# Kernel tuning notes

Measured on AMD Instinct MI355X. Metric: run time of the kernel, lower is better.

Reference implementation:

```python
import jax, jax.numpy as jnp
import numpy as np

N = 1_000_000
LIMS = ((0.0, 51.2), (-25.6, 25.6), (-2.0, 4.4))
SIZES = (256, 256, 32)
GM = np.array([0.2, 0.2, 0.2], np.float32)      # grid_meters
MINS = np.array([0.0, -25.6, -2.0], np.float32)  # xmin, ymin, zmin
OFFSET = 0.5
INIT = 32  # init_size; VFE units = INIT // 2 = 16


def setup_inputs() -> dict:
    key = jax.random.key(0)
    ks = jax.random.split(key, 20)
    lo = jnp.array([l[0] for l in LIMS], jnp.float32)
    hi = jnp.array([l[1] for l in LIMS], jnp.float32)
    # keep points strictly inside lims so quantized idx stays in range
    u = jax.random.uniform(ks[0], (N, 3), minval=1e-3, maxval=1.0 - 1e-3)
    xyz = lo + (hi - lo) * u
    inten = jax.random.uniform(ks[1], (N, 1))
    pc = jnp.concatenate([xyz, inten], axis=1).astype(jnp.float32)
    indicator = jnp.array([0, N // 2, N], jnp.int32)

    def lin(k, o, i):
        return (0.02 * jax.random.normal(k, (o, i), jnp.float32))

    def bias(k, o):
        return (0.02 * jax.random.normal(k, (o,), jnp.float32))

    U = INIT // 2  # 16, VFE units (last_vfe=False)
    return dict(
        pc=pc, indicator=indicator,
        w05=lin(ks[2], U, 10), b05=bias(ks[3], U),
        ww05=lin(ks[4], U, 6), wb05=bias(ks[5], U),
        w1=lin(ks[6], U, 10), b1=bias(ks[7], U),
        ww1=lin(ks[8], U, 6), wb1=bias(ks[9], U),
        am_w=lin(ks[10], INIT, 6), am_b=bias(ks[11], INIT),
        at_w=lin(ks[12], INIT, 2 * INIT), at_b=bias(ks[13], INIT),
        af_w=lin(ks[14], INIT, INIT), af_b=bias(ks[15], INIT),
    )


def _unique_inverse(ids):
    # emulate torch.unique(dim=0, return_inverse=True) via sort+rank on linear voxel ids
    n = ids.shape[0]
    order = jnp.argsort(ids)
    s = ids[order]
    new = jnp.concatenate([jnp.zeros((1,), jnp.int32), (s[1:] != s[:-1]).astype(jnp.int32)])
    ranks = jnp.cumsum(new)
    return jnp.zeros((n,), jnp.int32).at[order].set(ranks)


def _voxel_coords(pc, indicator, scale):
    n = pc.shape[0]
    B = indicator.shape[0] - 1
    bt = jnp.repeat(jnp.arange(B, dtype=jnp.int32), jnp.diff(indicator), total_repeat_length=n)
    nx = int(SIZES[0] // scale); ny = int(SIZES[1] // scale); nz = int(SIZES[2] // scale)
    def quant(col, lim, size):
        idx = (col - lim[0]) / (lim[1] - lim[0]) * float(size)
        return idx.astype(jnp.int32)
    xi = quant(pc[:, 0], LIMS[0], nx)
    yi = quant(pc[:, 1], LIMS[1], ny)
    zi = quant(pc[:, 2], LIMS[2], nz)
    coords = jnp.stack([bt, xi, yi, zi], axis=-1)  # [n,4] bxyz_indx
    lid = ((bt * nx + xi) * ny + yi) * nz + zi     # lexicographic-consistent linear id
    return coords, lid


def _scale_features(pc, coords, inv, Wl, bl, Ww, bw):
    # add_pcmean_and_gridmean + VFELayerMinus (activate=False, gs=None)
    n = pc.shape[0]
    cnt = jax.ops.segment_sum(jnp.ones((n,), jnp.float32), inv, num_segments=n)
    pc_mean = jax.ops.segment_sum(pc[:, :3], inv, num_segments=n) / jnp.maximum(cnt, 1.0)[:, None]
    mm = pc[:, :3] - pc_mean[inv]                                   # pc_mean_minus
    gm = jnp.asarray(GM); mins = jnp.asarray(MINS)
    gmm = pc[:, :3] - ((coords[:, 1:].astype(jnp.float32) + OFFSET) * gm + mins)  # pc_gridmean_minus
    feat = jnp.concatenate([pc, mm, gmm], axis=1)   # [n,10]
    mean = jnp.concatenate([mm, gmm], axis=1)       # [n,6]
    x = feat @ Wl.T + bl                            # [n,16]
    x = x * (mean @ Ww.T + bw)
    mx = jax.ops.segment_max(x, inv, num_segments=n)
    return jnp.concatenate([x, mx[inv]], axis=1), mean  # [n,32], [n,6]


def reference(pc, indicator, w05, b05, ww05, wb05, w1, b1, ww1, wb1,
              am_w, am_b, at_w, at_b, af_w, af_b):
    n = pc.shape[0]
    coords05, lid05 = _voxel_coords(pc, indicator, 0.5)
    coords1, lid1 = _voxel_coords(pc, indicator, 1)
    inv05 = _unique_inverse(lid05)
    inv1 = _unique_inverse(lid1)
    f05, _ = _scale_features(pc, coords05, inv05, w05, b05, ww05, wb05)
    f1, mean1 = _scale_features(pc, coords1, inv1, w1, b1, ww1, wb1)
    agg = jax.nn.relu(mean1 @ am_w.T + am_b) * \
          jax.nn.relu(jnp.concatenate([f05, f1], axis=1) @ at_w.T + at_b)
    agg = agg @ af_w.T + af_b                       # [n,32]
    maxf = jax.ops.segment_max(agg, inv1, num_segments=n)
    cnt = jax.ops.segment_sum(jnp.ones((n,), jnp.float32), inv1, num_segments=n)
    maxf = jnp.where(cnt[:, None] > 0, maxf, 0.0)   # pad empty rows (torch output has no such rows)
    coord_ind = jnp.zeros((n, 4), jnp.int32).at[inv1].set(coords1)  # unique coords, padded to n
    return maxf, coord_ind, inv1
```

## Files before the change

kernel.cpp:

```cpp
#include <hip/hip_runtime.h>
#include <cstdint>
#include <cstdio>


struct Coords { int xi, yi, zi; };

__device__ __forceinline__ Coords quantc(float x, float y, float z, float sx, float sy, float sz) {
    Coords c;
    c.xi = (int)(((x - 0.0f)  / 51.2f) * sx);
    c.yi = (int)(((y + 25.6f) / 51.2f) * sy);
    c.zi = (int)(((z + 2.0f)  / 6.4f)  * sz);
    return c;
}

__device__ __forceinline__ int batch_of(int i, const int* __restrict__ ind, int B) {
    int bt = 0;
    for (int b = 1; b < B; ++b) if (i >= ind[b]) bt = b;
    return bt;
}

__device__ __forceinline__ unsigned f2o(float f) {
    unsigned u = __float_as_uint(f);
    return (u & 0x80000000u) ? ~u : (u | 0x80000000u);
}
__device__ __forceinline__ float o2f(unsigned u) {
    return (u & 0x80000000u) ? __uint_as_float(u ^ 0x80000000u) : __uint_as_float(~u);
}
#define NEG_O 0x007FFFFFu

__device__ __forceinline__ unsigned short f2bf(float x) {
    unsigned u = __float_as_uint(x);
    unsigned r = (u + 0x7FFFu + ((u >> 16) & 1u)) >> 16;
    return (unsigned short)r;
}
__device__ __forceinline__ float bf2f(unsigned h) {
    return __uint_as_float(h << 16);
}

__device__ __forceinline__ void compute_x16(
    float px, float py, float pz, float pw,
    float mx_, float my_, float mz_, Coords c,
    const float* __restrict__ W, const float* __restrict__ Bv,
    const float* __restrict__ Ww, const float* __restrict__ Wb,
    float* __restrict__ x, float* __restrict__ mean6) {
    float gx = px - (((float)c.xi + 0.5f) * 0.2f + 0.0f);
    float gy = py - (((float)c.yi + 0.5f) * 0.2f + (-25.6f));
    float gz = pz - (((float)c.zi + 0.5f) * 0.2f + (-2.0f));
    float mmx = px - mx_, mmy = py - my_, mmz = pz - mz_;
    float feat[10] = {px, py, pz, pw, mmx, mmy, mmz, gx, gy, gz};
    float mean[6]  = {mmx, mmy, mmz, gx, gy, gz};
#pragma unroll
    for (int j = 0; j < 6; ++j) mean6[j] = mean[j];
#pragma unroll
    for (int o = 0; o < 16; ++o) {
        float a = Bv[o];
#pragma unroll
        for (int j = 0; j < 10; ++j) a += feat[j] * W[o * 10 + j];
        float g = Wb[o];
#pragma unroll
        for (int j = 0; j < 6; ++j) g += mean[j] * Ww[o * 6 + j];
        x[o] = a * g;
    }
}


__global__ __launch_bounds__(256) void k_bits(
    const float4* __restrict__ pc, const int* __restrict__ ind, int B, int n,
    unsigned* __restrict__ mask05, unsigned* __restrict__ mask1) {
    int i = blockIdx.x * 256 + threadIdx.x;
    if (i >= n) return;
    float4 p = pc[i];
    int bt = batch_of(i, ind, B);
    Coords c05 = quantc(p.x, p.y, p.z, 512.f, 512.f, 64.f);
    Coords c1  = quantc(p.x, p.y, p.z, 256.f, 256.f, 32.f);
    int lid05 = ((bt * 512 + c05.xi) * 512 + c05.yi) * 64 + c05.zi;
    int lid1  = ((bt * 256 + c1.xi)  * 256 + c1.yi)  * 32 + c1.zi;
    atomicOr(&mask05[lid05 >> 5], 1u << (lid05 & 31));
    atomicOr(&mask1[lid1 >> 5],  1u << (lid1 & 31));
}

__global__ __launch_bounds__(256) void k_wtr(
    const float* __restrict__ at_w, const float* __restrict__ af_w,
    const float* __restrict__ am_w,
    float* __restrict__ atT, float* __restrict__ afT, float* __restrict__ amT) {
    int i = blockIdx.x * 256 + threadIdx.x;
    if (i < 2048) {
        int o = i >> 6, c = i & 63;
        atT[c * 32 + o] = at_w[i];
    } else if (i < 3072) {
        int j = i - 2048; int o = j >> 5, q = j & 31;
        afT[q * 32 + o] = af_w[j];
    } else if (i < 3264) {
        int j = i - 3072; int o = j / 6, q = j % 6;
        amT[q * 32 + o] = am_w[j];
    }
}

__global__ __launch_bounds__(256) void k_chunk2(
    const unsigned* __restrict__ maskA, unsigned* __restrict__ bsumA, int nWA, int nBA,
    const unsigned* __restrict__ maskB, unsigned* __restrict__ bsumB, int nWB) {
    const unsigned* mask; unsigned* bsum; int nW, blk;
    if ((int)blockIdx.x < nBA) { mask = maskA; bsum = bsumA; nW = nWA; blk = blockIdx.x; }
    else { mask = maskB; bsum = bsumB; nW = nWB; blk = blockIdx.x - nBA; }
    int t = threadIdx.x;
    int base = blk * 2048 + t;
    unsigned tot = 0;
#pragma unroll
    for (int k = 0; k < 8; ++k) {
        int w = base + k * 256;
        if (w < nW) tot += __popc(mask[w]);
    }
    __shared__ unsigned s[256];
    s[t] = tot;
    __syncthreads();
    for (int off = 128; off > 0; off >>= 1) {
        if (t < off) s[t] += s[t + off];
        __syncthreads();
    }
    if (t == 0) bsum[blk] = s[0];
}

__global__ __launch_bounds__(256) void k_chunku2(
    const unsigned* __restrict__ cntA, unsigned* __restrict__ bsumA,
    const unsigned* __restrict__ cntB, unsigned* __restrict__ bsumB,
    int nElem, int nCh) {
    const unsigned* val; unsigned* bsum; int blk;
    if ((int)blockIdx.x < nCh) { val = cntA; bsum = bsumA; blk = blockIdx.x; }
    else { val = cntB; bsum = bsumB; blk = blockIdx.x - nCh; }
    int t = threadIdx.x;
    int base = blk * 2048 + t;
    unsigned tot = 0;
#pragma unroll
    for (int k = 0; k < 8; ++k) {
        int w = base + k * 256;
        if (w < nElem) tot += val[w];
    }
    __shared__ unsigned s[256];
    s[t] = tot;
    __syncthreads();
    for (int off = 128; off > 0; off >>= 1) {
        if (t < off) s[t] += s[t + off];
        __syncthreads();
    }
    if (t == 0) bsum[blk] = s[0];
}

__global__ __launch_bounds__(1024) void k_scan2(
    const unsigned* __restrict__ bsumA, unsigned* __restrict__ bprefA,
    unsigned* __restrict__ UoutA, int nA,
    const unsigned* __restrict__ bsumB, unsigned* __restrict__ bprefB,
    unsigned* __restrict__ UoutB, int nB) {
    const unsigned* bsum; unsigned* bpref; unsigned* Uout; int nBn;
    if (blockIdx.x == 0) { bsum = bsumA; bpref = bprefA; Uout = UoutA; nBn = nA; }
    else { bsum = bsumB; bpref = bprefB; Uout = UoutB; nBn = nB; }
    __shared__ unsigned s[1024];
    int t = threadIdx.x;
    int ipt = (nBn + 1023) >> 10;
    unsigned tot = 0;
    for (int k = 0; k < ipt; ++k) {
        int e = t * ipt + k;
        if (e < nBn) tot += bsum[e];
    }
    s[t] = tot;
    __syncthreads();
    for (int off = 1; off < 1024; off <<= 1) {
        unsigned v = 0;
        if (t >= off) v = s[t - off];
        __syncthreads();
        if (t >= off) s[t] += v;
        __syncthreads();
    }
    unsigned run = s[t] - tot;
    for (int k = 0; k < ipt; ++k) {
        int e = t * ipt + k;
        if (e < nBn) { bpref[e] = run; run += bsum[e]; }
    }
    if (t == 1023 && Uout) *Uout = s[1023];
}

__global__ __launch_bounds__(256) void k_wpref2(
    const unsigned* __restrict__ maskA, const unsigned* __restrict__ bprefA,
    unsigned* __restrict__ wprefA, int nWA, int nBA,
    const unsigned* __restrict__ maskB, const unsigned* __restrict__ bprefB,
    unsigned* __restrict__ wprefB, int nWB) {
    const unsigned* mask; const unsigned* bpref; unsigned* wpref; int nW, blk;
    if ((int)blockIdx.x < nBA) { mask = maskA; bpref = bprefA; wpref = wprefA; nW = nWA; blk = blockIdx.x; }
    else { mask = maskB; bpref = bprefB; wpref = wprefB; nW = nWB; blk = blockIdx.x - nBA; }
    int t = threadIdx.x;
    int base = blk * 2048 + t * 8;
    unsigned p[8];
    unsigned tot = 0;
#pragma unroll
    for (int k = 0; k < 8; ++k) {
        int w = base + k;
        p[k] = (w < nW) ? __popc(mask[w]) : 0u;
        tot += p[k];
    }
    __shared__ unsigned s[256];
    s[t] = tot;
    __syncthreads();
    for (int off = 1; off < 256; off <<= 1) {
        unsigned v = 0;
        if (t >= off) v = s[t - off];
        __syncthreads();
        if (t >= off) s[t] += v;
        __syncthreads();
    }
    unsigned run = bpref[blk] + (s[t] - tot);
#pragma unroll
    for (int k = 0; k < 8; ++k) {
        int w = base + k;
        if (w < nW) { wpref[w] = run; run += p[k]; }
    }
}

__global__ __launch_bounds__(256) void k_eprefu2(
    const unsigned* __restrict__ cntA, const unsigned* __restrict__ bprefA,
    unsigned* __restrict__ startA,
    const unsigned* __restrict__ cntB, const unsigned* __restrict__ bprefB,
    unsigned* __restrict__ startB,
    int nElem, int nCh) {
    const unsigned* val; const unsigned* bpref; unsigned* epref; int blk;
    if ((int)blockIdx.x < nCh) { val = cntA; bpref = bprefA; epref = startA; blk = blockIdx.x; }
    else { val = cntB; bpref = bprefB; epref = startB; blk = blockIdx.x - nCh; }
    int t = threadIdx.x;
    int base = blk * 2048 + t * 8;
    unsigned p[8];
    unsigned tot = 0;
#pragma unroll
    for (int k = 0; k < 8; ++k) {
        int w = base + k;
        p[k] = (w < nElem) ? val[w] : 0u;
        tot += p[k];
    }
    __shared__ unsigned s[256];
    s[t] = tot;
    __syncthreads();
    for (int off = 1; off < 256; off <<= 1) {
        unsigned v = 0;
        if (t >= off) v = s[t - off];
        __syncthreads();
        if (t >= off) s[t] += v;
        __syncthreads();
    }
    unsigned run = bpref[blk] + (s[t] - tot);
#pragma unroll
    for (int k = 0; k < 8; ++k) {
        int w = base + k;
        if (w < nElem) { epref[w] = run; run += p[k]; }
    }
}


__global__ __launch_bounds__(256) void k_rank(
    const float4* __restrict__ pc, const int* __restrict__ ind, int B, int n,
    const unsigned* __restrict__ mask05, const unsigned* __restrict__ wp05,
    const unsigned* __restrict__ mask1, const unsigned* __restrict__ wp1,
    unsigned* __restrict__ inv05, unsigned* __restrict__ inv1,
    unsigned* __restrict__ cnt05, unsigned* __restrict__ cnt1,
    unsigned* __restrict__ slot05, unsigned* __restrict__ slot1,
    float* __restrict__ outCoord, float* __restrict__ outInv) {
    int i = blockIdx.x * 256 + threadIdx.x;
    if (i >= n) return;
    float4 p = pc[i];
    int bt = batch_of(i, ind, B);
    Coords c05 = quantc(p.x, p.y, p.z, 512.f, 512.f, 64.f);
    Coords c1  = quantc(p.x, p.y, p.z, 256.f, 256.f, 32.f);
    int lid05 = ((bt * 512 + c05.xi) * 512 + c05.yi) * 64 + c05.zi;
    int lid1  = ((bt * 256 + c1.xi)  * 256 + c1.yi)  * 32 + c1.zi;

    unsigned w = (unsigned)lid05 >> 5, b = (unsigned)lid05 & 31u;
    unsigned r05 = wp05[w] + __popc(mask05[w] & ((1u << b) - 1u));
    w = (unsigned)lid1 >> 5; b = (unsigned)lid1 & 31u;
    unsigned r1 = wp1[w] + __popc(mask1[w] & ((1u << b) - 1u));

    inv05[i] = r05;
    inv1[i] = r1;
    outInv[i] = (float)r1;

    slot05[i] = atomicAdd(&cnt05[r05], 1u);
    unsigned sl1 = atomicAdd(&cnt1[r1], 1u);
    slot1[i] = sl1;
    if (sl1 == 0u)
        ((float4*)outCoord)[r1] = make_float4((float)bt, (float)c1.xi, (float)c1.yi, (float)c1.zi);
}

__global__ __launch_bounds__(256) void k_slot(
    const float4* __restrict__ pc,
    const unsigned* __restrict__ inv05, const unsigned* __restrict__ inv1,
    const unsigned* __restrict__ slot05, const unsigned* __restrict__ slot1,
    const unsigned* __restrict__ start05, const unsigned* __restrict__ start1,
    const unsigned* __restrict__ cnt1,
    uint4* __restrict__ recA05, uint4* __restrict__ recA1, int n) {
    int i = blockIdx.x * 256 + threadIdx.x;
    if (i >= n) return;
    float4 p = pc[i];
    unsigned r05 = inv05[i], r1 = inv1[i];
    unsigned p05 = start05[r05] + slot05[i];
    unsigned s1 = start1[r1];
    unsigned p1  = s1 + slot1[i];
    unsigned c1 = cnt1[r1];
    unsigned cm = c1 < 257u ? c1 : 257u;
    unsigned meta = s1 | (cm << 23);
    uint4 pw = *(const uint4*)&p;
    recA05[(size_t)p05 * 2]     = pw;
    recA05[(size_t)p05 * 2 + 1] = make_uint4(r05, 0u, 0u, 0u);
    recA1[(size_t)p1 * 2]       = pw;
    recA1[(size_t)p1 * 2 + 1]   = make_uint4(r1, r05, meta, 0u);
}

__global__ __launch_bounds__(256) void k_segmean2(
    const uint4* __restrict__ recA05, const unsigned* __restrict__ start05,
    const unsigned* __restrict__ cnt05, float4* __restrict__ mean05,
    const uint4* __restrict__ recA1, const unsigned* __restrict__ start1,
    const unsigned* __restrict__ cnt1, float4* __restrict__ mean1,
    unsigned char* __restrict__ flags, unsigned* __restrict__ outMaxU,
    int n, int gpts) {
    if ((int)blockIdx.x >= 2 * gpts) {
        int blk3 = blockIdx.x - 2 * gpts;
        int b = blk3 * 256 + threadIdx.x + 1;
        if (b >= gpts) return;
        int j = b * 256;
        if (j >= n) return;
        unsigned r = recA1[(size_t)j * 2 + 1].x;
        if (start1[r] < (unsigned)j) {
            flags[r] = 1;
            unsigned* row = outMaxU + (size_t)r * 32;
#pragma unroll
            for (int o = 0; o < 32; ++o) row[o] = NEG_O;
        }
        return;
    }
    const uint4* recA; const unsigned* start; const unsigned* cnt;
    float4* meanOut; int blk;
    if ((int)blockIdx.x < gpts) {
        recA = recA05; start = start05; cnt = cnt05; meanOut = mean05; blk = blockIdx.x;
    } else {
        recA = recA1; start = start1; cnt = cnt1; meanOut = mean1; blk = blockIdx.x - gpts;
    }
    int j = blk * 256 + threadIdx.x;
    int lane = threadIdx.x & 63;
    bool live = j < n;
    unsigned r = 0xFFFFFFFFu;
    float sx = 0.f, sy = 0.f, sz = 0.f;
    if (live) {
        float4 p = *(const float4*)&recA[(size_t)j * 2];
        r = recA[(size_t)j * 2 + 1].x;
        sx = p.x; sy = p.y; sz = p.z;
    }
#pragma unroll
    for (int d = 1; d < 64; d <<= 1) {
        unsigned rn = (unsigned)__shfl_down((int)r, d);
        float ax = __shfl_down(sx, d);
        float ay = __shfl_down(sy, d);
        float az = __shfl_down(sz, d);
        bool ok = (lane + d) < 64 && rn == r;
        if (ok) { sx += ax; sy += ay; sz += az; }
    }
    if (!live) return;
    if (j != (int)start[r]) return;
    unsigned c = cnt[r];
    unsigned end = j + c;
    unsigned waveEnd = ((unsigned)j & ~63u) + 64u;
    for (unsigned j2 = waveEnd; j2 < end; ++j2) {
        float4 q = *(const float4*)&recA[(size_t)j2 * 2];
        sx += q.x; sy += q.y; sz += q.z;
    }
    float cf = (float)c;
    meanOut[r] = make_float4(sx / cf, sy / cf, sz / cf, 0.f);
}

__global__ __launch_bounds__(256) void k_segmx2(
    const uint4* __restrict__ recA05, const unsigned* __restrict__ start05,
    const unsigned* __restrict__ cnt05, const float4* __restrict__ mean05,
    const float* __restrict__ w05, const float* __restrict__ b05,
    const float* __restrict__ ww05, const float* __restrict__ wb05,
    unsigned short* __restrict__ mx05,
    const uint4* __restrict__ recA1, const unsigned* __restrict__ start1,
    const unsigned* __restrict__ cnt1, const float4* __restrict__ mean1,
    const float* __restrict__ w1, const float* __restrict__ b1,
    const float* __restrict__ ww1, const float* __restrict__ wb1,
    unsigned short* __restrict__ mx1,
    int n, int gpts) {
    const uint4* recA; const unsigned* start; const unsigned* cnt;
    const float4* meanIn; const float* W; const float* Bv; const float* Ww;
    const float* Wb; unsigned short* mxOut; int blk;
    float sx_, sy_, sz_;
    if ((int)blockIdx.x < gpts) {
        recA = recA05; start = start05; cnt = cnt05; meanIn = mean05;
        W = w05; Bv = b05; Ww = ww05; Wb = wb05; mxOut = mx05;
        sx_ = 512.f; sy_ = 512.f; sz_ = 64.f; blk = blockIdx.x;
    } else {
        recA = recA1; start = start1; cnt = cnt1; meanIn = mean1;
        W = w1; Bv = b1; Ww = ww1; Wb = wb1; mxOut = mx1;
        sx_ = 256.f; sy_ = 256.f; sz_ = 32.f; blk = blockIdx.x - gpts;
    }
    __shared__ float buf[256][17];
    int t = threadIdx.x;
    int j = blk * 256 + t;
    bool live = j < n;
    unsigned r = 0;
    float x[16], d6[6];
    if (live) {
        float4 p = *(const float4*)&recA[(size_t)j * 2];
        r = recA[(size_t)j * 2 + 1].x;
        float4 mv = meanIn[r];
        Coords cc = quantc(p.x, p.y, p.z, sx_, sy_, sz_);
        compute_x16(p.x, p.y, p.z, p.w, mv.x, mv.y, mv.z, cc, W, Bv, Ww, Wb, x, d6);
    } else {
#pragma unroll
        for (int o = 0; o < 16; ++o) x[o] = 0.f;
    }
#pragma unroll
    for (int o = 0; o < 16; ++o) buf[t][o] = x[o];
    __syncthreads();
    if (!live || j != (int)start[r]) return;
    unsigned c = cnt[r];
    unsigned end = j + c;
    unsigned blockEnd = ((unsigned)blk + 1u) * 256u;
    unsigned inEnd = end < blockEnd ? end : blockEnd;
    for (unsigned j2 = j + 1; j2 < inEnd; ++j2) {
        int t2 = t + (int)(j2 - (unsigned)j);
#pragma unroll
        for (int o = 0; o < 16; ++o) x[o] = fmaxf(x[o], buf[t2][o]);
    }
    float4 mv = meanIn[r];
    for (unsigned j2 = blockEnd; j2 < end; ++j2) {
        float4 q = *(const float4*)&recA[(size_t)j2 * 2];
        Coords cc = quantc(q.x, q.y, q.z, sx_, sy_, sz_);
        float x2[16];
        compute_x16(q.x, q.y, q.z, q.w, mv.x, mv.y, mv.z, cc, W, Bv, Ww, Wb, x2, d6);
#pragma unroll
        for (int o = 0; o < 16; ++o) x[o] = fmaxf(x[o], x2[o]);
    }
    unsigned pk[8];
#pragma unroll
    for (int k = 0; k < 8; ++k)
        pk[k] = (unsigned)f2bf(x[2 * k]) | ((unsigned)f2bf(x[2 * k + 1]) << 16);
    uint4* mr = (uint4*)(mxOut + (size_t)r * 16);
    mr[0] = make_uint4(pk[0], pk[1], pk[2], pk[3]);
    mr[1] = make_uint4(pk[4], pk[5], pk[6], pk[7]);
}

__global__ __launch_bounds__(256, 3) void k_val(
    const uint4* __restrict__ recA1,
    const float4* __restrict__ mean05, const unsigned short* __restrict__ mx05,
    const float4* __restrict__ mean1, const unsigned short* __restrict__ mx1,
    const float* __restrict__ w05, const float* __restrict__ b05,
    const float* __restrict__ ww05, const float* __restrict__ wb05,
    const float* __restrict__ w1g, const float* __restrict__ b1g,
    const float* __restrict__ ww1, const float* __restrict__ wb1,
    const float* __restrict__ amT, const float* __restrict__ am_b,
    const float* __restrict__ atT, const float* __restrict__ at_b,
    const float* __restrict__ afT, const float* __restrict__ af_b,
    float* __restrict__ outMax, int n) {
    __shared__ float buf[256][17];
    int t = threadIdx.x;
    int j = blockIdx.x * 256 + t;
    bool live = j < n;
    unsigned r = 0, s = 0, c = 0;
    bool bound = false;
    float2 at2[16];
    if (live) {
        uint4 pw4 = recA1[(size_t)j * 2];
        float4 p = *(const float4*)&pw4;
        uint4 mw = recA1[(size_t)j * 2 + 1];
        r = mw.x;
        unsigned r05 = mw.y;
        unsigned meta = mw.z;
        s = meta & 0x7FFFFFu;
        c = meta >> 23;
        bound = (c > 256u) || ((s >> 8) != ((s + c - 1) >> 8));

#pragma unroll
        for (int k = 0; k < 16; ++k) at2[k] = ((const float2*)at_b)[k];

        {
            const uint4* m4 = (const uint4*)(mx1 + (size_t)r * 16);
            uint4 a = m4[0], b2 = m4[1];
            unsigned pw[8] = {a.x, a.y, a.z, a.w, b2.x, b2.y, b2.z, b2.w};
#pragma unroll
            for (int kk = 0; kk < 8; ++kk) {
                float e0 = bf2f(pw[kk] & 0xFFFFu);
                float e1 = bf2f(pw[kk] >> 16);
                const float2* wc0 = (const float2*)(atT + (48 + 2 * kk) * 32);
                const float2* wc1 = (const float2*)(atT + (49 + 2 * kk) * 32);
#pragma unroll
                for (int k = 0; k < 16; ++k) {
                    float2 w0 = wc0[k], w1 = wc1[k];
                    at2[k].x += e0 * w0.x + e1 * w1.x;
                    at2[k].y += e0 * w0.y + e1 * w1.y;
                }
            }
        }
        {
            const uint4* m4 = (const uint4*)(mx05 + (size_t)r05 * 16);
            uint4 a = m4[0], b2 = m4[1];
            unsigned pw[8] = {a.x, a.y, a.z, a.w, b2.x, b2.y, b2.z, b2.w};
#pragma unroll
            for (int kk = 0; kk < 8; ++kk) {
                float e0 = bf2f(pw[kk] & 0xFFFFu);
                float e1 = bf2f(pw[kk] >> 16);
                const float2* wc0 = (const float2*)(atT + (16 + 2 * kk) * 32);
                const float2* wc1 = (const float2*)(atT + (17 + 2 * kk) * 32);
#pragma unroll
                for (int k = 0; k < 16; ++k) {
                    float2 w0 = wc0[k], w1 = wc1[k];
                    at2[k].x += e0 * w0.x + e1 * w1.x;
                    at2[k].y += e0 * w0.y + e1 * w1.y;
                }
            }
        }
        {
            float4 mv = mean05[r05];
            Coords cc = quantc(p.x, p.y, p.z, 512.f, 512.f, 64.f);
            float gx = p.x - (((float)cc.xi + 0.5f) * 0.1f + 0.0f);
            float gy = p.y - (((float)cc.yi + 0.5f) * 0.1f + (-25.6f));
            float gz = p.z - (((float)cc.zi + 0.5f) * 0.1f + (-2.0f));
            float mmx = p.x - mv.x, mmy = p.y - mv.y, mmz = p.z - mv.z;
            float feat[10] = {p.x, p.y, p.z, p.w, mmx, mmy, mmz, gx, gy, gz};
#pragma unroll
            for (int jj = 0; jj < 16; ++jj) {
                float a_ = b05[jj];
#pragma unroll
                for (int q = 0; q < 10; ++q) a_ += feat[q] * w05[jj * 10 + q];
                float g_ = wb05[jj];
#pragma unroll
                for (int q = 0; q < 6; ++q) g_ += feat[4 + q] * ww05[jj * 6 + q];
                float x_ = a_ * g_;
                const float2* wc = (const float2*)(atT + jj * 32);
#pragma unroll
                for (int k = 0; k < 16; ++k) {
                    float2 w0 = wc[k];
                    at2[k].x += x_ * w0.x;
                    at2[k].y += x_ * w0.y;
                }
            }
        }
        float mean6[6];
        {
            float4 mv = mean1[r];
            Coords cc = quantc(p.x, p.y, p.z, 256.f, 256.f, 32.f);
            float gx = p.x - (((float)cc.xi + 0.5f) * 0.2f + 0.0f);
            float gy = p.y - (((float)cc.yi + 0.5f) * 0.2f + (-25.6f));
            float gz = p.z - (((float)cc.zi + 0.5f) * 0.2f + (-2.0f));
            float mmx = p.x - mv.x, mmy = p.y - mv.y, mmz = p.z - mv.z;
            float feat[10] = {p.x, p.y, p.z, p.w, mmx, mmy, mmz, gx, gy, gz};
            mean6[0] = mmx; mean6[1] = mmy; mean6[2] = mmz;
            mean6[3] = gx;  mean6[4] = gy;  mean6[5] = gz;
#pragma unroll
            for (int jj = 0; jj < 16; ++jj) {
                float a_ = b1g[jj];
#pragma unroll
                for (int q = 0; q < 10; ++q) a_ += feat[q] * w1g[jj * 10 + q];
                float g_ = wb1[jj];
#pragma unroll
                for (int q = 0; q < 6; ++q) g_ += feat[4 + q] * ww1[jj * 6 + q];
                float x_ = a_ * g_;
                const float2* wc = (const float2*)(atT + (32 + jj) * 32);
#pragma unroll
                for (int k = 0; k < 16; ++k) {
                    float2 w0 = wc[k];
                    at2[k].x += x_ * w0.x;
                    at2[k].y += x_ * w0.y;
                }
            }
        }
        {
            float2 am2[16];
#pragma unroll
            for (int k = 0; k < 16; ++k) am2[k] = ((const float2*)am_b)[k];
#pragma unroll
            for (int q = 0; q < 6; ++q) {
                float m = mean6[q];
                const float2* wc = (const float2*)(amT + q * 32);
#pragma unroll
                for (int k = 0; k < 16; ++k) {
                    float2 w0 = wc[k];
                    am2[k].x += m * w0.x;
                    am2[k].y += m * w0.y;
                }
            }
#pragma unroll
            for (int k = 0; k < 16; ++k) {
                at2[k].x = fmaxf(am2[k].x, 0.f) * fmaxf(at2[k].x, 0.f);
                at2[k].y = fmaxf(am2[k].y, 0.f) * fmaxf(at2[k].y, 0.f);
            }
        }
    } else {
#pragma unroll
        for (int k = 0; k < 16; ++k) at2[k] = make_float2(0.f, 0.f);
    }

    float ats[32];
#pragma unroll
    for (int k = 0; k < 16; ++k) { ats[2 * k] = at2[k].x; ats[2 * k + 1] = at2[k].y; }

    bool owner = live && !bound && (j == (int)s);
    unsigned end = s + c;
    unsigned* arow = (unsigned*)outMax + (size_t)r * 32;
    float4* ov = (float4*)(outMax + (size_t)r * 32);

    if (live) {
#pragma unroll
        for (int k = 0; k < 8; ++k) {
            float2 v2 = ((const float2*)af_b)[k];
#pragma unroll
            for (int q = 0; q < 32; ++q) {
                float aq = ats[q];
                float2 w2 = ((const float2*)(afT + q * 32))[k];
                v2.x += aq * w2.x;
                v2.y += aq * w2.y;
            }
            if (bound) {
                atomicMax(&arow[2 * k], f2o(v2.x));
                atomicMax(&arow[2 * k + 1], f2o(v2.y));
            } else {
                buf[t][2 * k] = v2.x;
                buf[t][2 * k + 1] = v2.y;
            }
        }
    }
    __syncthreads();
    if (owner) {
        float vm[16];
#pragma unroll
        for (int o = 0; o < 16; ++o) vm[o] = buf[t][o];
        for (unsigned j2 = (unsigned)j + 1; j2 < end; ++j2) {
            int t2 = t + (int)(j2 - (unsigned)j);
#pragma unroll
            for (int o = 0; o < 16; ++o) vm[o] = fmaxf(vm[o], buf[t2][o]);
        }
#pragma unroll
        for (int k = 0; k < 4; ++k)
            ov[k] = make_float4(vm[4 * k], vm[4 * k + 1], vm[4 * k + 2], vm[4 * k + 3]);
    }
    __syncthreads();
    if (live) {
#pragma unroll
        for (int k = 8; k < 16; ++k) {
            float2 v2 = ((const float2*)af_b)[k];
#pragma unroll
            for (int q = 0; q < 32; ++q) {
                float aq = ats[q];
                float2 w2 = ((const float2*)(afT + q * 32))[k];
                v2.x += aq * w2.x;
                v2.y += aq * w2.y;
            }
            if (bound) {
                atomicMax(&arow[2 * k], f2o(v2.x));
                atomicMax(&arow[2 * k + 1], f2o(v2.y));
            } else {
                buf[t][2 * (k - 8)] = v2.x;
                buf[t][2 * (k - 8) + 1] = v2.y;
            }
        }
    }
    __syncthreads();
    if (owner) {
        float vm[16];
#pragma unroll
        for (int o = 0; o < 16; ++o) vm[o] = buf[t][o];
        for (unsigned j2 = (unsigned)j + 1; j2 < end; ++j2) {
            int t2 = t + (int)(j2 - (unsigned)j);
#pragma unroll
            for (int o = 0; o < 16; ++o) vm[o] = fmaxf(vm[o], buf[t2][o]);
        }
#pragma unroll
        for (int k = 0; k < 4; ++k)
            ov[4 + k] = make_float4(vm[4 * k], vm[4 * k + 1], vm[4 * k + 2], vm[4 * k + 3]);
    }
}

__global__ __launch_bounds__(256) void k_finrow(
    float* __restrict__ outMax, float* __restrict__ outCoord,
    const unsigned char* __restrict__ flags, const unsigned* __restrict__ U1p, int n) {
    int idx = blockIdx.x * 256 + threadIdx.x;
    if (idx >= n * 8) return;
    int r = idx >> 3, k = idx & 7;
    unsigned U = *U1p;
    if ((unsigned)r >= U) {
        float4 z = make_float4(0.f, 0.f, 0.f, 0.f);
        ((float4*)outMax)[idx] = z;
        if (k == 0) ((float4*)outCoord)[r] = z;
    } else if (flags[r]) {
        unsigned* u4 = (unsigned*)outMax + (size_t)idx * 4;
        float* f4 = outMax + (size_t)idx * 4;
#pragma unroll
        for (int o = 0; o < 4; ++o) f4[o] = o2f(u4[o]);
    }
}


extern "C" void kernel_launch(void* const* d_in, const int* in_sizes, int n_in,
                              void* d_out, int out_size, void* d_ws, size_t ws_size,
                              hipStream_t stream) {
    const float4* pc = (const float4*)d_in[0];
    const int* ind   = (const int*)d_in[1];
    const float* w05 = (const float*)d_in[2];
    const float* b05 = (const float*)d_in[3];
    const float* ww05 = (const float*)d_in[4];
    const float* wb05 = (const float*)d_in[5];
    const float* w1  = (const float*)d_in[6];
    const float* b1  = (const float*)d_in[7];
    const float* ww1 = (const float*)d_in[8];
    const float* wb1 = (const float*)d_in[9];
    const float* am_w = (const float*)d_in[10];
    const float* am_b = (const float*)d_in[11];
    const float* at_w = (const float*)d_in[12];
    const float* at_b = (const float*)d_in[13];
    const float* af_w = (const float*)d_in[14];
    const float* af_b = (const float*)d_in[15];

    int n = in_sizes[0] / 4;
    int B = in_sizes[1] - 1;

    int nW05 = B * (512 * 512 * 64 / 32);
    int nW1  = B * (256 * 256 * 32 / 32);
    int nB05 = (nW05 + 2047) / 2048;
    int nB1  = (nW1 + 2047) / 2048;
    int nCh  = (n + 2047) / 2048;

    size_t off = 0;
    char* base = (char*)d_ws;
    auto take = [&](size_t bytes) -> char* {
        char* p = base + off;
        off = (off + bytes + 255) & ~(size_t)255;
        return p;
    };

    unsigned* mask05 = (unsigned*)take((size_t)nW05 * 4);
    unsigned* mask1  = (unsigned*)take((size_t)nW1 * 4);
    unsigned* cnt05  = (unsigned*)take((size_t)n * 4);
    unsigned* cnt1   = (unsigned*)take((size_t)n * 4);
    unsigned char* flags = (unsigned char*)take((size_t)n);
    size_t zeroBytes = off;

    unsigned* wp05   = (unsigned*)take((size_t)nW05 * 4);
    unsigned* wp1    = (unsigned*)take((size_t)nW1 * 4);
    unsigned* inv05  = (unsigned*)take((size_t)n * 4);
    unsigned* inv1   = (unsigned*)take((size_t)n * 4);
    unsigned* slot05 = (unsigned*)take((size_t)n * 4);
    unsigned* slot1  = (unsigned*)take((size_t)n * 4);
    unsigned* start05 = (unsigned*)take((size_t)n * 4);
    unsigned* start1  = (unsigned*)take((size_t)n * 4);
    uint4*    recA05  = (uint4*)take((size_t)n * 32);
    uint4*    recA1   = (uint4*)take((size_t)n * 32);
    float4*   mean05  = (float4*)take((size_t)n * 16);
    float4*   mean1   = (float4*)take((size_t)n * 16);
    unsigned short* mx05 = (unsigned short*)take((size_t)n * 32);
    unsigned short* mx1  = (unsigned short*)take((size_t)n * 32);
    float*    atT     = (float*)take((size_t)2048 * 4);
    float*    afT     = (float*)take((size_t)1024 * 4);
    float*    amT     = (float*)take((size_t)192 * 4);
    unsigned* bsum05  = (unsigned*)take((size_t)nB05 * 4);
    unsigned* bpref05 = (unsigned*)take((size_t)nB05 * 4);
    unsigned* bsum1   = (unsigned*)take((size_t)nB1 * 4);
    unsigned* bpref1  = (unsigned*)take((size_t)nB1 * 4);
    unsigned* bsC05   = (unsigned*)take((size_t)nCh * 4);
    unsigned* bpC05   = (unsigned*)take((size_t)nCh * 4);
    unsigned* bsC1    = (unsigned*)take((size_t)nCh * 4);
    unsigned* bpC1    = (unsigned*)take((size_t)nCh * 4);
    unsigned* U1p     = (unsigned*)take(4);
    size_t total = off;

    if (ws_size < total) {
        fprintf(stderr, "kernel_launch: ws too small (%zu < %zu)\n", ws_size, total);
        return;
    }

    float* outMaxF = (float*)d_out;
    float* outCoord = (float*)d_out + (size_t)n * 32;
    float* outInv = (float*)d_out + (size_t)n * 36;

    hipMemsetAsync(d_ws, 0, zeroBytes, stream);

    int gpts = (n + 255) / 256;
    int nbb  = (gpts + 255) / 256;
    k_wtr<<<13, 256, 0, stream>>>(at_w, af_w, am_w, atT, afT, amT);
    k_bits<<<gpts, 256, 0, stream>>>(pc, ind, B, n, mask05, mask1);
    k_chunk2<<<nB05 + nB1, 256, 0, stream>>>(mask05, bsum05, nW05, nB05,
                                             mask1, bsum1, nW1);
    k_scan2<<<2, 1024, 0, stream>>>(bsum05, bpref05, nullptr, nB05,
                                    bsum1, bpref1, U1p, nB1);
    k_wpref2<<<nB05 + nB1, 256, 0, stream>>>(mask05, bpref05, wp05, nW05, nB05,
                                             mask1, bpref1, wp1, nW1);
    k_rank<<<gpts, 256, 0, stream>>>(pc, ind, B, n, mask05, wp05, mask1, wp1,
                                     inv05, inv1, cnt05, cnt1, slot05, slot1,
                                     outCoord, outInv);
    k_chunku2<<<2 * nCh, 256, 0, stream>>>(cnt05, bsC05, cnt1, bsC1, n, nCh);
    k_scan2<<<2, 1024, 0, stream>>>(bsC05, bpC05, nullptr, nCh,
                                    bsC1, bpC1, nullptr, nCh);
    k_eprefu2<<<2 * nCh, 256, 0, stream>>>(cnt05, bpC05, start05,
                                           cnt1, bpC1, start1, n, nCh);
    k_slot<<<gpts, 256, 0, stream>>>(pc, inv05, inv1, slot05, slot1,
                                     start05, start1, cnt1, recA05, recA1, n);
    k_segmean2<<<2 * gpts + nbb, 256, 0, stream>>>(recA05, start05, cnt05, mean05,
                                                   recA1, start1, cnt1, mean1,
                                                   flags, (unsigned*)outMaxF, n, gpts);
    k_segmx2<<<2 * gpts, 256, 0, stream>>>(recA05, start05, cnt05, mean05,
                                           w05, b05, ww05, wb05, mx05,
                                           recA1, start1, cnt1, mean1,
                                           w1, b1, ww1, wb1, mx1, n, gpts);
    k_val<<<gpts, 256, 0, stream>>>(recA1,
                                    mean05, mx05, mean1, mx1,
                                    w05, b05, ww05, wb05, w1, b1, ww1, wb1,
                                    amT, am_b, atT, at_b, afT, af_b,
                                    outMaxF, n);
    k_finrow<<<(n * 8 + 255) / 256, 256, 0, stream>>>(outMaxF, outCoord, flags, U1p, n);

    (void)n_in; (void)out_size;
}
```

Baseline: 702.2 us.

## Transpose VFE weights, interleave mask with prefix, fold weight transpose into bits kernel

Transposes the small VFE weight matrices so the per-point 16-output linear layers read float2 pairs along the output dimension, shared through a new vfe_pair helper. The word prefix and mask word are stored together as uint2 so the rank lookup needs one 8-byte load instead of two separate loads. The standalone weight-transpose kernel is merged into extra blocks of the bitmask kernel, removing one launch. The cost is a larger prefix array and extra transposed-weight buffers.

```diff
diff --git a/kernel.cpp b/kernel.cpp
--- a/kernel.cpp
+++ b/kernel.cpp
@@ -37,36 +37,54 @@
     return __uint_as_float(h << 16);
 }
 
-__device__ __forceinline__ void compute_x16(
-    float px, float py, float pz, float pw,
-    float mx_, float my_, float mz_, Coords c,
-    const float* __restrict__ W, const float* __restrict__ Bv,
-    const float* __restrict__ Ww, const float* __restrict__ Wb,
-    float* __restrict__ x, float* __restrict__ mean6) {
-    float gx = px - (((float)c.xi + 0.5f) * 0.2f + 0.0f);
-    float gy = py - (((float)c.yi + 0.5f) * 0.2f + (-25.6f));
-    float gz = pz - (((float)c.zi + 0.5f) * 0.2f + (-2.0f));
-    float mmx = px - mx_, mmy = py - my_, mmz = pz - mz_;
-    float feat[10] = {px, py, pz, pw, mmx, mmy, mmz, gx, gy, gz};
-    float mean[6]  = {mmx, mmy, mmz, gx, gy, gz};
-#pragma unroll
-    for (int j = 0; j < 6; ++j) mean6[j] = mean[j];
-#pragma unroll
-    for (int o = 0; o < 16; ++o) {
-        float a = Bv[o];
-#pragma unroll
-        for (int j = 0; j < 10; ++j) a += feat[j] * W[o * 10 + j];
-        float g = Wb[o];
-#pragma unroll
-        for (int j = 0; j < 6; ++j) g += mean[j] * Ww[o * 6 + j];
-        x[o] = a * g;
+__device__ __forceinline__ void vfe_pair(
+    const float* __restrict__ feat,
+    const float* __restrict__ WT, const float* __restrict__ Bv,
+    const float* __restrict__ WwT, const float* __restrict__ Wb,
+    float* __restrict__ x) {
+#pragma unroll
+    for (int k8 = 0; k8 < 8; ++k8) {
+        float2 a2 = ((const float2*)Bv)[k8];
+        float2 g2 = ((const float2*)Wb)[k8];
+#pragma unroll
+        for (int q = 0; q < 10; ++q) {
+            float2 w2 = ((const float2*)(WT + q * 16))[k8];
+            a2.x += feat[q] * w2.x;
+            a2.y += feat[q] * w2.y;
+        }
+#pragma unroll
+        for (int q = 0; q < 6; ++q) {
+            float2 w2 = ((const float2*)(WwT + q * 16))[k8];
+            g2.x += feat[4 + q] * w2.x;
+            g2.y += feat[4 + q] * w2.y;
+        }
+        x[2 * k8] = a2.x * g2.x;
+        x[2 * k8 + 1] = a2.y * g2.y;
     }
 }
 
 
 __global__ __launch_bounds__(256) void k_bits(
-    const float4* __restrict__ pc, const int* __restrict__ ind, int B, int n,
-    unsigned* __restrict__ mask05, unsigned* __restrict__ mask1) {
+    const float4* __restrict__ pc, const int* __restrict__ ind, int B, int n, int gpts,
+    unsigned* __restrict__ mask05, unsigned* __restrict__ mask1,
+    const float* __restrict__ at_w, const float* __restrict__ af_w,
+    const float* __restrict__ am_w,
+    const float* __restrict__ w05, const float* __restrict__ ww05,
+    const float* __restrict__ w1, const float* __restrict__ ww1,
+    float* __restrict__ atT, float* __restrict__ afT, float* __restrict__ amT,
+    float* __restrict__ w05T, float* __restrict__ ww05T,
+    float* __restrict__ w1T, float* __restrict__ ww1T) {
+    if ((int)blockIdx.x >= gpts) {
+        int i = (blockIdx.x - gpts) * 256 + threadIdx.x;
+        if (i < 2048) { int o = i >> 6, c2 = i & 63; atT[c2 * 32 + o] = at_w[i]; }
+        else if (i < 3072) { int j2 = i - 2048; int o = j2 >> 5, q = j2 & 31; afT[q * 32 + o] = af_w[j2]; }
+        else if (i < 3264) { int j2 = i - 3072; int o = j2 / 6, q = j2 % 6; amT[q * 32 + o] = am_w[j2]; }
+        else if (i < 3424) { int j2 = i - 3264; int o = j2 / 10, q = j2 % 10; w05T[q * 16 + o] = w05[j2]; }
+        else if (i < 3520) { int j2 = i - 3424; int o = j2 / 6, q = j2 % 6; ww05T[q * 16 + o] = ww05[j2]; }
+        else if (i < 3680) { int j2 = i - 3520; int o = j2 / 10, q = j2 % 10; w1T[q * 16 + o] = w1[j2]; }
+        else if (i < 3776) { int j2 = i - 3680; int o = j2 / 6, q = j2 % 6; ww1T[q * 16 + o] = ww1[j2]; }
+        return;
+    }
     int i = blockIdx.x * 256 + threadIdx.x;
     if (i >= n) return;
     float4 p = pc[i];
@@ -77,23 +95,6 @@
     int lid1  = ((bt * 256 + c1.xi)  * 256 + c1.yi)  * 32 + c1.zi;
     atomicOr(&mask05[lid05 >> 5], 1u << (lid05 & 31));
     atomicOr(&mask1[lid1 >> 5],  1u << (lid1 & 31));
-}
-
-__global__ __launch_bounds__(256) void k_wtr(
-    const float* __restrict__ at_w, const float* __restrict__ af_w,
-    const float* __restrict__ am_w,
-    float* __restrict__ atT, float* __restrict__ afT, float* __restrict__ amT) {
-    int i = blockIdx.x * 256 + threadIdx.x;
-    if (i < 2048) {
-        int o = i >> 6, c = i & 63;
-        atT[c * 32 + o] = at_w[i];
-    } else if (i < 3072) {
-        int j = i - 2048; int o = j >> 5, q = j & 31;
-        afT[q * 32 + o] = af_w[j];
-    } else if (i < 3264) {
-        int j = i - 3072; int o = j / 6, q = j % 6;
-        amT[q * 32 + o] = am_w[j];
-    }
 }
 
 __global__ __launch_bounds__(256) void k_chunk2(
@@ -180,20 +181,22 @@
 
 __global__ __launch_bounds__(256) void k_wpref2(
     const unsigned* __restrict__ maskA, const unsigned* __restrict__ bprefA,
-    unsigned* __restrict__ wprefA, int nWA, int nBA,
+    uint2* __restrict__ mwA, int nWA, int nBA,
     const unsigned* __restrict__ maskB, const unsigned* __restrict__ bprefB,
-    unsigned* __restrict__ wprefB, int nWB) {
-    const unsigned* mask; const unsigned* bpref; unsigned* wpref; int nW, blk;
-    if ((int)blockIdx.x < nBA) { mask = maskA; bpref = bprefA; wpref = wprefA; nW = nWA; blk = blockIdx.x; }
-    else { mask = maskB; bpref = bprefB; wpref = wprefB; nW = nWB; blk = blockIdx.x - nBA; }
+    uint2* __restrict__ mwB, int nWB) {
+    const unsigned* mask; const unsigned* bpref; uint2* mw; int nW, blk;
+    if ((int)blockIdx.x < nBA) { mask = maskA; bpref = bprefA; mw = mwA; nW = nWA; blk = blockIdx.x; }
+    else { mask = maskB; bpref = bprefB; mw = mwB; nW = nWB; blk = blockIdx.x - nBA; }
     int t = threadIdx.x;
     int base = blk * 2048 + t * 8;
+    unsigned m[8];
     unsigned p[8];
     unsigned tot = 0;
 #pragma unroll
     for (int k = 0; k < 8; ++k) {
         int w = base + k;
-        p[k] = (w < nW) ? __popc(mask[w]) : 0u;
+        m[k] = (w < nW) ? mask[w] : 0u;
+        p[k] = __popc(m[k]);
         tot += p[k];
     }
     __shared__ unsigned s[256];
@@ -210,7 +213,7 @@
 #pragma unroll
     for (int k = 0; k < 8; ++k) {
         int w = base + k;
-        if (w < nW) { wpref[w] = run; run += p[k]; }
+        if (w < nW) { mw[w] = make_uint2(run, m[k]); run += p[k]; }
     }
 }
 
@@ -254,8 +257,7 @@
 
 __global__ __launch_bounds__(256) void k_rank(
     const float4* __restrict__ pc, const int* __restrict__ ind, int B, int n,
-    const unsigned* __restrict__ mask05, const unsigned* __restrict__ wp05,
-    const unsigned* __restrict__ mask1, const unsigned* __restrict__ wp1,
+    const uint2* __restrict__ mw05, const uint2* __restrict__ mw1,
     unsigned* __restrict__ inv05, unsigned* __restrict__ inv1,
     unsigned* __restrict__ cnt05, unsigned* __restrict__ cnt1,
     unsigned* __restrict__ slot05, unsigned* __restrict__ slot1,
@@ -269,10 +271,10 @@
     int lid05 = ((bt * 512 + c05.xi) * 512 + c05.yi) * 64 + c05.zi;
     int lid1  = ((bt * 256 + c1.xi)  * 256 + c1.yi)  * 32 + c1.zi;
 
-    unsigned w = (unsigned)lid05 >> 5, b = (unsigned)lid05 & 31u;
-    unsigned r05 = wp05[w] + __popc(mask05[w] & ((1u << b) - 1u));
-    w = (unsigned)lid1 >> 5; b = (unsigned)lid1 & 31u;
-    unsigned r1 = wp1[w] + __popc(mask1[w] & ((1u << b) - 1u));
+    uint2 a05 = mw05[(unsigned)lid05 >> 5];
+    unsigned r05 = a05.x + __popc(a05.y & ((1u << ((unsigned)lid05 & 31u)) - 1u));
+    uint2 a1 = mw1[(unsigned)lid1 >> 5];
+    unsigned r1 = a1.x + __popc(a1.y & ((1u << ((unsigned)lid1 & 31u)) - 1u));
 
     inv05[i] = r05;
     inv1[i] = r1;
@@ -373,26 +375,26 @@
 __global__ __launch_bounds__(256) void k_segmx2(
     const uint4* __restrict__ recA05, const unsigned* __restrict__ start05,
     const unsigned* __restrict__ cnt05, const float4* __restrict__ mean05,
-    const float* __restrict__ w05, const float* __restrict__ b05,
-    const float* __restrict__ ww05, const float* __restrict__ wb05,
+    const float* __restrict__ w05T, const float* __restrict__ b05,
+    const float* __restrict__ ww05T, const float* __restrict__ wb05,
     unsigned short* __restrict__ mx05,
     const uint4* __restrict__ recA1, const unsigned* __restrict__ start1,
     const unsigned* __restrict__ cnt1, const float4* __restrict__ mean1,
-    const float* __restrict__ w1, const float* __restrict__ b1,
-    const float* __restrict__ ww1, const float* __restrict__ wb1,
+    const float* __restrict__ w1T, const float* __restrict__ b1,
+    const float* __restrict__ ww1T, const float* __restrict__ wb1,
     unsigned short* __restrict__ mx1,
     int n, int gpts) {
     const uint4* recA; const unsigned* start; const unsigned* cnt;
-    const float4* meanIn; const float* W; const float* Bv; const float* Ww;
+    const float4* meanIn; const float* WT; const float* Bv; const float* WwT;
     const float* Wb; unsigned short* mxOut; int blk;
     float sx_, sy_, sz_;
     if ((int)blockIdx.x < gpts) {
         recA = recA05; start = start05; cnt = cnt05; meanIn = mean05;
-        W = w05; Bv = b05; Ww = ww05; Wb = wb05; mxOut = mx05;
+        WT = w05T; Bv = b05; WwT = ww05T; Wb = wb05; mxOut = mx05;
         sx_ = 512.f; sy_ = 512.f; sz_ = 64.f; blk = blockIdx.x;
     } else {
         recA = recA1; start = start1; cnt = cnt1; meanIn = mean1;
-        W = w1; Bv = b1; Ww = ww1; Wb = wb1; mxOut = mx1;
+        WT = w1T; Bv = b1; WwT = ww1T; Wb = wb1; mxOut = mx1;
         sx_ = 256.f; sy_ = 256.f; sz_ = 32.f; blk = blockIdx.x - gpts;
     }
     __shared__ float buf[256][17];
@@ -400,13 +402,18 @@
     int j = blk * 256 + t;
     bool live = j < n;
     unsigned r = 0;
-    float x[16], d6[6];
+    float x[16];
     if (live) {
         float4 p = *(const float4*)&recA[(size_t)j * 2];
         r = recA[(size_t)j * 2 + 1].x;
         float4 mv = meanIn[r];
         Coords cc = quantc(p.x, p.y, p.z, sx_, sy_, sz_);
-        compute_x16(p.x, p.y, p.z, p.w, mv.x, mv.y, mv.z, cc, W, Bv, Ww, Wb, x, d6);
+        float gx = p.x - (((float)cc.xi + 0.5f) * 0.2f + 0.0f);
+        float gy = p.y - (((float)cc.yi + 0.5f) * 0.2f + (-25.6f));
+        float gz = p.z - (((float)cc.zi + 0.5f) * 0.2f + (-2.0f));
+        float feat[10] = {p.x, p.y, p.z, p.w,
+                          p.x - mv.x, p.y - mv.y, p.z - mv.z, gx, gy, gz};
+        vfe_pair(feat, WT, Bv, WwT, Wb, x);
     } else {
 #pragma unroll
         for (int o = 0; o < 16; ++o) x[o] = 0.f;
@@ -428,8 +435,13 @@
     for (unsigned j2 = blockEnd; j2 < end; ++j2) {
         float4 q = *(const float4*)&recA[(size_t)j2 * 2];
         Coords cc = quantc(q.x, q.y, q.z, sx_, sy_, sz_);
+        float gx = q.x - (((float)cc.xi + 0.5f) * 0.2f + 0.0f);
+        float gy = q.y - (((float)cc.yi + 0.5f) * 0.2f + (-25.6f));
+        float gz = q.z - (((float)cc.zi + 0.5f) * 0.2f + (-2.0f));
+        float feat[10] = {q.x, q.y, q.z, q.w,
+                          q.x - mv.x, q.y - mv.y, q.z - mv.z, gx, gy, gz};
         float x2[16];
-        compute_x16(q.x, q.y, q.z, q.w, mv.x, mv.y, mv.z, cc, W, Bv, Ww, Wb, x2, d6);
+        vfe_pair(feat, WT, Bv, WwT, Wb, x2);
 #pragma unroll
         for (int o = 0; o < 16; ++o) x[o] = fmaxf(x[o], x2[o]);
     }
@@ -446,10 +458,10 @@
     const uint4* __restrict__ recA1,
     const float4* __restrict__ mean05, const unsigned short* __restrict__ mx05,
     const float4* __restrict__ mean1, const unsigned short* __restrict__ mx1,
-    const float* __restrict__ w05, const float* __restrict__ b05,
-    const float* __restrict__ ww05, const float* __restrict__ wb05,
-    const float* __restrict__ w1g, const float* __restrict__ b1g,
-    const float* __restrict__ ww1, const float* __restrict__ wb1,
+    const float* __restrict__ w05T, const float* __restrict__ b05,
+    const float* __restrict__ ww05T, const float* __restrict__ wb05,
+    const float* __restrict__ w1T, const float* __restrict__ b1g,
+    const float* __restrict__ ww1T, const float* __restrict__ wb1,
     const float* __restrict__ amT, const float* __restrict__ am_b,
     const float* __restrict__ atT, const float* __restrict__ at_b,
     const float* __restrict__ afT, const float* __restrict__ af_b,
@@ -517,17 +529,13 @@
             float gx = p.x - (((float)cc.xi + 0.5f) * 0.1f + 0.0f);
             float gy = p.y - (((float)cc.yi + 0.5f) * 0.1f + (-25.6f));
             float gz = p.z - (((float)cc.zi + 0.5f) * 0.1f + (-2.0f));
-            float mmx = p.x - mv.x, mmy = p.y - mv.y, mmz = p.z - mv.z;
-            float feat[10] = {p.x, p.y, p.z, p.w, mmx, mmy, mmz, gx, gy, gz};
+            float feat[10] = {p.x, p.y, p.z, p.w,
+                              p.x - mv.x, p.y - mv.y, p.z - mv.z, gx, gy, gz};
+            float xv[16];
+            vfe_pair(feat, w05T, b05, ww05T, wb05, xv);
 #pragma unroll
             for (int jj = 0; jj < 16; ++jj) {
-                float a_ = b05[jj];
-#pragma unroll
-                for (int q = 0; q < 10; ++q) a_ += feat[q] * w05[jj * 10 + q];
-                float g_ = wb05[jj];
-#pragma unroll
-                for (int q = 0; q < 6; ++q) g_ += feat[4 + q] * ww05[jj * 6 + q];
-                float x_ = a_ * g_;
+                float x_ = xv[jj];
                 const float2* wc = (const float2*)(atT + jj * 32);
 #pragma unroll
                 for (int k = 0; k < 16; ++k) {
@@ -544,19 +552,15 @@
             float gx = p.x - (((float)cc.xi + 0.5f) * 0.2f + 0.0f);
             float gy = p.y - (((float)cc.yi + 0.5f) * 0.2f + (-25.6f));
             float gz = p.z - (((float)cc.zi + 0.5f) * 0.2f + (-2.0f));
-            float mmx = p.x - mv.x, mmy = p.y - mv.y, mmz = p.z - mv.z;
-            float feat[10] = {p.x, p.y, p.z, p.w, mmx, mmy, mmz, gx, gy, gz};
-            mean6[0] = mmx; mean6[1] = mmy; mean6[2] = mmz;
+            float feat[10] = {p.x, p.y, p.z, p.w,
+                              p.x - mv.x, p.y - mv.y, p.z - mv.z, gx, gy, gz};
+            mean6[0] = feat[4]; mean6[1] = feat[5]; mean6[2] = feat[6];
             mean6[3] = gx;  mean6[4] = gy;  mean6[5] = gz;
+            float xv[16];
+            vfe_pair(feat, w1T, b1g, ww1T, wb1, xv);
 #pragma unroll
             for (int jj = 0; jj < 16; ++jj) {
-                float a_ = b1g[jj];
-#pragma unroll
-                for (int q = 0; q < 10; ++q) a_ += feat[q] * w1g[jj * 10 + q];
-                float g_ = wb1[jj];
-#pragma unroll
-                for (int q = 0; q < 6; ++q) g_ += feat[4 + q] * ww1[jj * 6 + q];
-                float x_ = a_ * g_;
+                float x_ = xv[jj];
                 const float2* wc = (const float2*)(atT + (32 + jj) * 32);
 #pragma unroll
                 for (int k = 0; k < 16; ++k) {
@@ -736,8 +740,8 @@
     unsigned char* flags = (unsigned char*)take((size_t)n);
     size_t zeroBytes = off;
 
-    unsigned* wp05   = (unsigned*)take((size_t)nW05 * 4);
-    unsigned* wp1    = (unsigned*)take((size_t)nW1 * 4);
+    uint2*    mw05   = (uint2*)take((size_t)nW05 * 8);
+    uint2*    mw1    = (uint2*)take((size_t)nW1 * 8);
     unsigned* inv05  = (unsigned*)take((size_t)n * 4);
     unsigned* inv1   = (unsigned*)take((size_t)n * 4);
     unsigned* slot05 = (unsigned*)take((size_t)n * 4);
@@ -753,6 +757,10 @@
     float*    atT     = (float*)take((size_t)2048 * 4);
     float*    afT     = (float*)take((size_t)1024 * 4);
     float*    amT     = (float*)take((size_t)192 * 4);
+    float*    w05T    = (float*)take((size_t)160 * 4);
+    float*    ww05T   = (float*)take((size_t)96 * 4);
+    float*    w1T     = (float*)take((size_t)160 * 4);
+    float*    ww1T    = (float*)take((size_t)96 * 4);
     unsigned* bsum05  = (unsigned*)take((size_t)nB05 * 4);
     unsigned* bpref05 = (unsigned*)take((size_t)nB05 * 4);
     unsigned* bsum1   = (unsigned*)take((size_t)nB1 * 4);
@@ -777,15 +785,16 @@
 
     int gpts = (n + 255) / 256;
     int nbb  = (gpts + 255) / 256;
-    k_wtr<<<13, 256, 0, stream>>>(at_w, af_w, am_w, atT, afT, amT);
-    k_bits<<<gpts, 256, 0, stream>>>(pc, ind, B, n, mask05, mask1);
+    k_bits<<<gpts + 15, 256, 0, stream>>>(pc, ind, B, n, gpts, mask05, mask1,
+                                          at_w, af_w, am_w, w05, ww05, w1, ww1,
+                                          atT, afT, amT, w05T, ww05T, w1T, ww1T);
     k_chunk2<<<nB05 + nB1, 256, 0, stream>>>(mask05, bsum05, nW05, nB05,
                                              mask1, bsum1, nW1);
     k_scan2<<<2, 1024, 0, stream>>>(bsum05, bpref05, nullptr, nB05,
                                     bsum1, bpref1, U1p, nB1);
-    k_wpref2<<<nB05 + nB1, 256, 0, stream>>>(mask05, bpref05, wp05, nW05, nB05,
-                                             mask1, bpref1, wp1, nW1);
-    k_rank<<<gpts, 256, 0, stream>>>(pc, ind, B, n, mask05, wp05, mask1, wp1,
+    k_wpref2<<<nB05 + nB1, 256, 0, stream>>>(mask05, bpref05, mw05, nW05, nB05,
+                                             mask1, bpref1, mw1, nW1);
+    k_rank<<<gpts, 256, 0, stream>>>(pc, ind, B, n, mw05, mw1,
                                      inv05, inv1, cnt05, cnt1, slot05, slot1,
                                      outCoord, outInv);
     k_chunku2<<<2 * nCh, 256, 0, stream>>>(cnt05, bsC05, cnt1, bsC1, n, nCh);
@@ -799,12 +808,12 @@
                                                    recA1, start1, cnt1, mean1,
                                                    flags, (unsigned*)outMaxF, n, gpts);
     k_segmx2<<<2 * gpts, 256, 0, stream>>>(recA05, start05, cnt05, mean05,
-                                           w05, b05, ww05, wb05, mx05,
+                                           w05T, b05, ww05T, wb05, mx05,
                                            recA1, start1, cnt1, mean1,
-                                           w1, b1, ww1, wb1, mx1, n, gpts);
+                                           w1T, b1, ww1T, wb1, mx1, n, gpts);
     k_val<<<gpts, 256, 0, stream>>>(recA1,
                                     mean05, mx05, mean1, mx1,
-                                    w05, b05, ww05, wb05, w1, b1, ww1, wb1,
+                                    w05T, b05, ww05T, wb05, w1T, b1, ww1T, wb1,
                                     amT, am_b, atT, at_b, afT, af_b,
                                     outMaxF, n);
     k_finrow<<<(n * 8 + 255) / 256, 256, 0, stream>>>(outMaxF, outCoord, flags, U1p, n);
```

After: 903.0 us. 28.6% more time.
